# Optimization experiments

Measured on AMD Instinct MI355X. Metric: run time of the kernel, lower is better.

Reference implementation:

```python
import jax, jax.numpy as jnp
import numpy as np

HIDDEN = 512
OUTPUT = 256
TIMESTEPS = 16
THRESH = 0.5


def setup_inputs() -> dict:
    key = jax.random.key(0)
    k_x, k_w1, k_b1, k_w2, k_b2 = jax.random.split(key, 5)
    B, S, IN = 16, 2048, 512
    x = jax.random.normal(k_x, (B, S, IN), dtype=jnp.float32)
    # nn.Linear default init: U(-1/sqrt(fan_in), 1/sqrt(fan_in))
    lim1 = 1.0 / np.sqrt(IN)
    W1 = jax.random.uniform(k_w1, (HIDDEN, IN), minval=-lim1, maxval=lim1, dtype=jnp.float32)
    b1 = jax.random.uniform(k_b1, (HIDDEN,), minval=-lim1, maxval=lim1, dtype=jnp.float32)
    lim2 = 1.0 / np.sqrt(HIDDEN)
    W2 = jax.random.uniform(k_w2, (OUTPUT, HIDDEN), minval=-lim2, maxval=lim2, dtype=jnp.float32)
    b2 = jax.random.uniform(k_b2, (OUTPUT,), minval=-lim2, maxval=lim2, dtype=jnp.float32)
    return {"x": x, "W1": W1, "b1": b1, "W2": W2, "b2": b2}


def reference(x, W1, b1, W2, b2):
    # fc1(x) is the same every timestep (x is constant) -> compute once.
    pre1 = jnp.einsum("bsi,hi->bsh", x, W1) + b1  # [B,S,H]
    B, S, _ = pre1.shape
    mem1 = jnp.zeros((B, S, HIDDEN), dtype=x.dtype)
    mem2 = jnp.zeros((B, S, OUTPUT), dtype=x.dtype)
    spike_sum = jnp.zeros((B, S, OUTPUT), dtype=x.dtype)

    def step(carry, _):
        mem1, mem2, acc = carry
        mem1 = mem1 + pre1
        spike1 = (mem1 > THRESH).astype(x.dtype)
        mem1 = mem1 * (mem1 <= THRESH).astype(x.dtype)
        # dropout p=0.0 -> identity
        mem2 = mem2 + jnp.einsum("bsh,oh->bso", spike1, W2) + b2
        spike2 = (mem2 > THRESH).astype(x.dtype)
        mem2 = mem2 * (mem2 <= THRESH).astype(x.dtype)
        return (mem1, mem2, acc + spike2), None

    (mem1, mem2, spike_sum), _ = jax.lax.scan(
        step, (mem1, mem2, spike_sum), None, length=TIMESTEPS
    )
    return spike_sum / TIMESTEPS  # mean over timesteps, [B,S,OUTPUT]
```

## Files before the change

### kernel.cpp

```cpp
#include <hip/hip_runtime.h>
#include <cstdint>

#define NPOS 32768
#define IND  512
#define HID  512
#define OUTF 256

typedef float v2f __attribute__((ext_vector_type(2)));

__global__ __launch_bounds__(256) void k_transpose(const float* __restrict__ W2,
                                                   float* __restrict__ w2t) {
  __shared__ float tile[32][33];
  int x = threadIdx.x & 31, y = threadIdx.x >> 5;
  int hb = blockIdx.x * 32, ob = blockIdx.y * 32;
#pragma unroll
  for (int dy = 0; dy < 32; dy += 8)
    tile[y + dy][x] = W2[(size_t)(ob + y + dy) * HID + hb + x];
  __syncthreads();
#pragma unroll
  for (int dy = 0; dy < 32; dy += 8)
    w2t[(size_t)(hb + y + dy) * OUTF + ob + x] = tile[x][y + dy];
}

__global__ __launch_bounds__(256) void k_fc1_kmap(const float* __restrict__ X,
                                                  const float* __restrict__ W1,
                                                  const float* __restrict__ b1,
                                                  unsigned char* __restrict__ kmap) {
  __shared__ float As[8][128];
  __shared__ float Bs[8][128];
  const int row0 = blockIdx.x * 128;
  const int col0 = blockIdx.y * 128;
  const int t = threadIdx.x;
  const int tm0 = (t & 15) * 8;
  const int tn0 = (t >> 4) * 8;

  float c[8][8];
#pragma unroll
  for (int i = 0; i < 8; ++i)
#pragma unroll
    for (int j = 0; j < 8; ++j) c[i][j] = 0.0f;

  const int sm = t >> 1;
  const int sk = (t & 1) * 4;

  for (int kt = 0; kt < IND; kt += 8) {
    float4 va = *(const float4*)(X + (size_t)(row0 + sm) * IND + kt + sk);
    float4 vb = *(const float4*)(W1 + (size_t)(col0 + sm) * IND + kt + sk);
    __syncthreads();
    As[sk + 0][sm] = va.x; As[sk + 1][sm] = va.y;
    As[sk + 2][sm] = va.z; As[sk + 3][sm] = va.w;
    Bs[sk + 0][sm] = vb.x; Bs[sk + 1][sm] = vb.y;
    Bs[sk + 2][sm] = vb.z; Bs[sk + 3][sm] = vb.w;
    __syncthreads();
#pragma unroll
    for (int kk = 0; kk < 8; ++kk) {
      float4 a0 = *(const float4*)&As[kk][tm0];
      float4 a1 = *(const float4*)&As[kk][tm0 + 4];
      float4 b0 = *(const float4*)&Bs[kk][tn0];
      float4 b1_ = *(const float4*)&Bs[kk][tn0 + 4];
      float a[8] = {a0.x, a0.y, a0.z, a0.w, a1.x, a1.y, a1.z, a1.w};
      float b[8] = {b0.x, b0.y, b0.z, b0.w, b1_.x, b1_.y, b1_.z, b1_.w};
#pragma unroll
      for (int i = 0; i < 8; ++i)
#pragma unroll
        for (int j = 0; j < 8; ++j)
          c[i][j] = __fadd_rn(c[i][j], __fmul_rn(a[i], b[j]));
    }
  }

  float4 b1a = *(const float4*)(b1 + col0 + tn0);
  float4 b1b = *(const float4*)(b1 + col0 + tn0 + 4);
  float b1v[8] = {b1a.x, b1a.y, b1a.z, b1a.w, b1b.x, b1b.y, b1b.z, b1b.w};

#pragma unroll
  for (int i = 0; i < 8; ++i) {
    unsigned long long pk = 0;
#pragma unroll
    for (int j = 0; j < 8; ++j) {
      float pre = __fadd_rn(c[i][j], b1v[j]);
      float m = 0.0f;
      int kv = 0;
#pragma unroll
      for (int tt = 1; tt <= 16; ++tt) {
        m = __fadd_rn(m, pre);
        if (m > 0.5f && kv == 0) kv = tt;
      }
      pk |= (unsigned long long)(unsigned int)kv << (8 * j);
    }
    *(unsigned long long*)(kmap + (size_t)(row0 + tm0 + i) * HID + col0 + tn0) = pk;
  }
}

__global__ __launch_bounds__(128) void k_snn_fc2(const unsigned char* __restrict__ kmap,
                                                 const float* __restrict__ w2t,
                                                 const float* __restrict__ b2,
                                                 float* __restrict__ out) {
  const int tid = threadIdx.x;
  const size_t pos = blockIdx.x;

  v2f a1 = {0.f, 0.f}, a2 = a1, a3 = a1, a4 = a1, a5 = a1, a6 = a1,
      a7 = a1, a8 = a1, a9 = a1, a10 = a1, a11 = a1, a12 = a1,
      a13 = a1, a14 = a1, a15 = a1, a16 = a1;

  const uint4* kp = (const uint4*)(kmap + pos * HID);
  const v2f* w2p = (const v2f*)w2t;

#define PK(acc) asm volatile("v_pk_add_f32 %0, %0, %1" : "+v"(acc) : "v"(w))

#define DO_H(HB, KB)                                                      \
  do {                                                                    \
    int k_ = (int)(KB);                                                   \
    if (k_) {                                                             \
      v2f w = w2p[(size_t)(HB) * 128 + tid];                              \
      switch (k_) {                                                       \
        case 1:                                                           \
          PK(a1);  PK(a2);  PK(a3);  PK(a4);                              \
          PK(a5);  PK(a6);  PK(a7);  PK(a8);                              \
          PK(a9);  PK(a10); PK(a11); PK(a12);                             \
          PK(a13); PK(a14); PK(a15); PK(a16);                             \
          break;                                                          \
        case 2:                                                           \
          PK(a2);  PK(a4);  PK(a6);  PK(a8);                              \
          PK(a10); PK(a12); PK(a14); PK(a16);                             \
          break;                                                          \
        case 3:  PK(a3); PK(a6); PK(a9); PK(a12); PK(a15); break;         \
        case 4:  PK(a4); PK(a8); PK(a12); PK(a16); break;                 \
        case 5:  PK(a5); PK(a10); PK(a15); break;                         \
        case 6:  PK(a6); PK(a12); break;                                  \
        case 7:  PK(a7); PK(a14); break;                                  \
        case 8:  PK(a8); PK(a16); break;                                  \
        case 9:  PK(a9); break;                                           \
        case 10: PK(a10); break;                                          \
        case 11: PK(a11); break;                                          \
        case 12: PK(a12); break;                                          \
        case 13: PK(a13); break;                                          \
        case 14: PK(a14); break;                                          \
        case 15: PK(a15); break;                                          \
        default: PK(a16); break;                             \
      }                                                                   \
    }                                                                     \
  } while (0)

  for (int it = 0; it < 32; ++it) {
    uint4 kw = kp[it];
    int hb = it * 16;
    {
      unsigned uw = __builtin_amdgcn_readfirstlane(kw.x);
      DO_H(hb + 0, uw & 255u);         DO_H(hb + 1, (uw >> 8) & 255u);
      DO_H(hb + 2, (uw >> 16) & 255u); DO_H(hb + 3, uw >> 24);
    }
    {
      unsigned uw = __builtin_amdgcn_readfirstlane(kw.y);
      DO_H(hb + 4, uw & 255u);         DO_H(hb + 5, (uw >> 8) & 255u);
      DO_H(hb + 6, (uw >> 16) & 255u); DO_H(hb + 7, uw >> 24);
    }
    {
      unsigned uw = __builtin_amdgcn_readfirstlane(kw.z);
      DO_H(hb + 8, uw & 255u);          DO_H(hb + 9, (uw >> 8) & 255u);
      DO_H(hb + 10, (uw >> 16) & 255u); DO_H(hb + 11, uw >> 24);
    }
    {
      unsigned uw = __builtin_amdgcn_readfirstlane(kw.w);
      DO_H(hb + 12, uw & 255u);         DO_H(hb + 13, (uw >> 8) & 255u);
      DO_H(hb + 14, (uw >> 16) & 255u); DO_H(hb + 15, uw >> 24);
    }
  }
#undef DO_H
#undef PK

  v2f b2v = *(const v2f*)(b2 + 2 * tid);
  float memx = 0.0f, ssx = 0.0f, memy = 0.0f, ssy = 0.0f;
#define STEP(AT)                                              \
  do {                                                        \
    memx = __fadd_rn(__fadd_rn(memx, (AT).x), b2v.x);         \
    if (memx > 0.5f) { ssx += 1.0f; memx = 0.0f; }            \
    memy = __fadd_rn(__fadd_rn(memy, (AT).y), b2v.y);         \
    if (memy > 0.5f) { ssy += 1.0f; memy = 0.0f; }            \
  } while (0)
  STEP(a1);  STEP(a2);  STEP(a3);  STEP(a4);
  STEP(a5);  STEP(a6);  STEP(a7);  STEP(a8);
  STEP(a9);  STEP(a10); STEP(a11); STEP(a12);
  STEP(a13); STEP(a14); STEP(a15); STEP(a16);
#undef STEP
  v2f r = {ssx * 0.0625f, ssy * 0.0625f};
  *(v2f*)(out + pos * OUTF + 2 * tid) = r;
}

extern "C" void kernel_launch(void* const* d_in, const int* in_sizes, int n_in,
                              void* d_out, int out_size, void* d_ws, size_t ws_size,
                              hipStream_t stream) {
  const float* X  = (const float*)d_in[0];
  const float* W1 = (const float*)d_in[1];
  const float* b1 = (const float*)d_in[2];
  const float* W2 = (const float*)d_in[3];
  const float* b2 = (const float*)d_in[4];
  float* out = (float*)d_out;

  float* w2t = (float*)d_ws;
  unsigned char* kmap = (unsigned char*)d_ws + (size_t)HID * OUTF * 4;

  k_transpose<<<dim3(16, 8), 256, 0, stream>>>(W2, w2t);
  k_fc1_kmap<<<dim3(256, 4), 256, 0, stream>>>(X, W1, b1, kmap);
  k_snn_fc2<<<NPOS, 128, 0, stream>>>(kmap, w2t, b2, out);
}
```

Before: 1.461 ms.

## Stage W2 chunks in LDS shared by eight positions per block

The fc2 spike-accumulation kernel now handles eight positions per 512-thread block, one wave per position, with each lane covering four outputs. W2^T is staged into shared memory in 64-row chunks so the eight waves reuse it instead of each re-reading it from global or L2. This adds block-wide barriers and a 64KB LDS footprint, which limits occupancy, and it doubles the accumulator registers per lane.

```diff
diff --git a/kernel.cpp b/kernel.cpp
--- a/kernel.cpp
+++ b/kernel.cpp
@@ -91,99 +91,130 @@
   }
 }
 
-__global__ __launch_bounds__(128) void k_snn_fc2(const unsigned char* __restrict__ kmap,
+__global__ __launch_bounds__(512) void k_snn_fc2(const unsigned char* __restrict__ kmap,
                                                  const float* __restrict__ w2t,
                                                  const float* __restrict__ b2,
                                                  float* __restrict__ out) {
+  __shared__ float w2s[64 * 256];
   const int tid = threadIdx.x;
-  const size_t pos = blockIdx.x;
-
-  v2f a1 = {0.f, 0.f}, a2 = a1, a3 = a1, a4 = a1, a5 = a1, a6 = a1,
-      a7 = a1, a8 = a1, a9 = a1, a10 = a1, a11 = a1, a12 = a1,
-      a13 = a1, a14 = a1, a15 = a1, a16 = a1;
-
-  const uint4* kp = (const uint4*)(kmap + pos * HID);
-  const v2f* w2p = (const v2f*)w2t;
-
-#define PK(acc) asm volatile("v_pk_add_f32 %0, %0, %1" : "+v"(acc) : "v"(w))
-
-#define DO_H(HB, KB)                                                      \
+  const int wave = tid >> 6;
+  const int lane = tid & 63;
+  const size_t pos = (size_t)blockIdx.x * 8 + wave;
+
+  v2f z = {0.f, 0.f};
+  v2f a1l = z, a2l = z, a3l = z, a4l = z, a5l = z, a6l = z, a7l = z, a8l = z,
+      a9l = z, a10l = z, a11l = z, a12l = z, a13l = z, a14l = z, a15l = z, a16l = z;
+  v2f a1h = z, a2h = z, a3h = z, a4h = z, a5h = z, a6h = z, a7h = z, a8h = z,
+      a9h = z, a10h = z, a11h = z, a12h = z, a13h = z, a14h = z, a15h = z, a16h = z;
+
+  const v2f* wp = (const v2f*)w2s;
+
+#define PK2(accl, acch)                                                   \
+  do {                                                                    \
+    asm volatile("v_pk_add_f32 %0, %0, %1" : "+v"(accl) : "v"(wlo));      \
+    asm volatile("v_pk_add_f32 %0, %0, %1" : "+v"(acch) : "v"(whi));      \
+  } while (0)
+
+#define DO_H(HL, KB)                                                      \
   do {                                                                    \
     int k_ = (int)(KB);                                                   \
     if (k_) {                                                             \
-      v2f w = w2p[(size_t)(HB) * 128 + tid];                              \
+      v2f wlo = wp[(HL) * 128 + lane * 2];                                \
+      v2f whi = wp[(HL) * 128 + lane * 2 + 1];                            \
       switch (k_) {                                                       \
         case 1:                                                           \
-          PK(a1);  PK(a2);  PK(a3);  PK(a4);                              \
-          PK(a5);  PK(a6);  PK(a7);  PK(a8);                              \
-          PK(a9);  PK(a10); PK(a11); PK(a12);                             \
-          PK(a13); PK(a14); PK(a15); PK(a16);                             \
+          PK2(a1l, a1h);  PK2(a2l, a2h);  PK2(a3l, a3h);  PK2(a4l, a4h);  \
+          PK2(a5l, a5h);  PK2(a6l, a6h);  PK2(a7l, a7h);  PK2(a8l, a8h);  \
+          PK2(a9l, a9h);  PK2(a10l, a10h); PK2(a11l, a11h); PK2(a12l, a12h);\
+          PK2(a13l, a13h); PK2(a14l, a14h); PK2(a15l, a15h); PK2(a16l, a16h);\
           break;                                                          \
         case 2:                                                           \
-          PK(a2);  PK(a4);  PK(a6);  PK(a8);                              \
-          PK(a10); PK(a12); PK(a14); PK(a16);                             \
+          PK2(a2l, a2h);  PK2(a4l, a4h);  PK2(a6l, a6h);  PK2(a8l, a8h);  \
+          PK2(a10l, a10h); PK2(a12l, a12h); PK2(a14l, a14h); PK2(a16l, a16h);\
           break;                                                          \
-        case 3:  PK(a3); PK(a6); PK(a9); PK(a12); PK(a15); break;         \
-        case 4:  PK(a4); PK(a8); PK(a12); PK(a16); break;                 \
-        case 5:  PK(a5); PK(a10); PK(a15); break;                         \
-        case 6:  PK(a6); PK(a12); break;                                  \
-        case 7:  PK(a7); PK(a14); break;                                  \
-        case 8:  PK(a8); PK(a16); break;                                  \
-        case 9:  PK(a9); break;                                           \
-        case 10: PK(a10); break;                                          \
-        case 11: PK(a11); break;                                          \
-        case 12: PK(a12); break;                                          \
-        case 13: PK(a13); break;                                          \
-        case 14: PK(a14); break;                                          \
-        case 15: PK(a15); break;                                          \
-        default: PK(a16); break;                             \
+        case 3:                                                           \
+          PK2(a3l, a3h); PK2(a6l, a6h); PK2(a9l, a9h); PK2(a12l, a12h);   \
+          PK2(a15l, a15h); break;                                         \
+        case 4:                                                           \
+          PK2(a4l, a4h); PK2(a8l, a8h); PK2(a12l, a12h); PK2(a16l, a16h); \
+          break;                                                          \
+        case 5:  PK2(a5l, a5h); PK2(a10l, a10h); PK2(a15l, a15h); break;  \
+        case 6:  PK2(a6l, a6h); PK2(a12l, a12h); break;                   \
+        case 7:  PK2(a7l, a7h); PK2(a14l, a14h); break;                   \
+        case 8:  PK2(a8l, a8h); PK2(a16l, a16h); break;                   \
+        case 9:  PK2(a9l, a9h); break;                                    \
+        case 10: PK2(a10l, a10h); break;                                  \
+        case 11: PK2(a11l, a11h); break;                                  \
+        case 12: PK2(a12l, a12h); break;                                  \
+        case 13: PK2(a13l, a13h); break;                                  \
+        case 14: PK2(a14l, a14h); break;                                  \
+        case 15: PK2(a15l, a15h); break;                                  \
+        default: PK2(a16l, a16h); break;                     \
       }                                                                   \
     }                                                                     \
   } while (0)
 
-  for (int it = 0; it < 32; ++it) {
-    uint4 kw = kp[it];
-    int hb = it * 16;
-    {
-      unsigned uw = __builtin_amdgcn_readfirstlane(kw.x);
-      DO_H(hb + 0, uw & 255u);         DO_H(hb + 1, (uw >> 8) & 255u);
-      DO_H(hb + 2, (uw >> 16) & 255u); DO_H(hb + 3, uw >> 24);
-    }
-    {
-      unsigned uw = __builtin_amdgcn_readfirstlane(kw.y);
-      DO_H(hb + 4, uw & 255u);         DO_H(hb + 5, (uw >> 8) & 255u);
-      DO_H(hb + 6, (uw >> 16) & 255u); DO_H(hb + 7, uw >> 24);
-    }
-    {
-      unsigned uw = __builtin_amdgcn_readfirstlane(kw.z);
-      DO_H(hb + 8, uw & 255u);          DO_H(hb + 9, (uw >> 8) & 255u);
-      DO_H(hb + 10, (uw >> 16) & 255u); DO_H(hb + 11, uw >> 24);
-    }
-    {
-      unsigned uw = __builtin_amdgcn_readfirstlane(kw.w);
-      DO_H(hb + 12, uw & 255u);         DO_H(hb + 13, (uw >> 8) & 255u);
-      DO_H(hb + 14, (uw >> 16) & 255u); DO_H(hb + 15, uw >> 24);
+  for (int ch = 0; ch < 8; ++ch) {
+    __syncthreads();
+    const float4* src = (const float4*)(w2t + (size_t)ch * 64 * 256);
+#pragma unroll
+    for (int j = 0; j < 8; ++j) {
+      int fi = tid + j * 512;
+      ((float4*)w2s)[fi] = src[fi];
+    }
+    __syncthreads();
+
+    const uint4* kp = (const uint4*)(kmap + pos * HID + ch * 64);
+#pragma unroll
+    for (int q = 0; q < 4; ++q) {
+      uint4 kw = kp[q];
+      int hl = q * 16;
+      {
+        unsigned uw = __builtin_amdgcn_readfirstlane(kw.x);
+        DO_H(hl + 0, uw & 255u);         DO_H(hl + 1, (uw >> 8) & 255u);
+        DO_H(hl + 2, (uw >> 16) & 255u); DO_H(hl + 3, uw >> 24);
+      }
+      {
+        unsigned uw = __builtin_amdgcn_readfirstlane(kw.y);
+        DO_H(hl + 4, uw & 255u);         DO_H(hl + 5, (uw >> 8) & 255u);
+        DO_H(hl + 6, (uw >> 16) & 255u); DO_H(hl + 7, uw >> 24);
+      }
+      {
+        unsigned uw = __builtin_amdgcn_readfirstlane(kw.z);
+        DO_H(hl + 8, uw & 255u);          DO_H(hl + 9, (uw >> 8) & 255u);
+        DO_H(hl + 10, (uw >> 16) & 255u); DO_H(hl + 11, uw >> 24);
+      }
+      {
+        unsigned uw = __builtin_amdgcn_readfirstlane(kw.w);
+        DO_H(hl + 12, uw & 255u);         DO_H(hl + 13, (uw >> 8) & 255u);
+        DO_H(hl + 14, (uw >> 16) & 255u); DO_H(hl + 15, uw >> 24);
+      }
     }
   }
 #undef DO_H
-#undef PK
-
-  v2f b2v = *(const v2f*)(b2 + 2 * tid);
-  float memx = 0.0f, ssx = 0.0f, memy = 0.0f, ssy = 0.0f;
-#define STEP(AT)                                              \
+#undef PK2
+
+  float4 b2v = *(const float4*)(b2 + 4 * lane);
+  float m0 = 0.f, m1 = 0.f, m2 = 0.f, m3 = 0.f;
+  float s0 = 0.f, s1 = 0.f, s2 = 0.f, s3 = 0.f;
+#define STEP(AL, AH)                                          \
   do {                                                        \
-    memx = __fadd_rn(__fadd_rn(memx, (AT).x), b2v.x);         \
-    if (memx > 0.5f) { ssx += 1.0f; memx = 0.0f; }            \
-    memy = __fadd_rn(__fadd_rn(memy, (AT).y), b2v.y);         \
-    if (memy > 0.5f) { ssy += 1.0f; memy = 0.0f; }            \
+    m0 = __fadd_rn(__fadd_rn(m0, (AL).x), b2v.x);             \
+    if (m0 > 0.5f) { s0 += 1.0f; m0 = 0.0f; }                 \
+    m1 = __fadd_rn(__fadd_rn(m1, (AL).y), b2v.y);             \
+    if (m1 > 0.5f) { s1 += 1.0f; m1 = 0.0f; }                 \
+    m2 = __fadd_rn(__fadd_rn(m2, (AH).x), b2v.z);             \
+    if (m2 > 0.5f) { s2 += 1.0f; m2 = 0.0f; }                 \
+    m3 = __fadd_rn(__fadd_rn(m3, (AH).y), b2v.w);             \
+    if (m3 > 0.5f) { s3 += 1.0f; m3 = 0.0f; }                 \
   } while (0)
-  STEP(a1);  STEP(a2);  STEP(a3);  STEP(a4);
-  STEP(a5);  STEP(a6);  STEP(a7);  STEP(a8);
-  STEP(a9);  STEP(a10); STEP(a11); STEP(a12);
-  STEP(a13); STEP(a14); STEP(a15); STEP(a16);
+  STEP(a1l, a1h);   STEP(a2l, a2h);   STEP(a3l, a3h);   STEP(a4l, a4h);
+  STEP(a5l, a5h);   STEP(a6l, a6h);   STEP(a7l, a7h);   STEP(a8l, a8h);
+  STEP(a9l, a9h);   STEP(a10l, a10h); STEP(a11l, a11h); STEP(a12l, a12h);
+  STEP(a13l, a13h); STEP(a14l, a14h); STEP(a15l, a15h); STEP(a16l, a16h);
 #undef STEP
-  v2f r = {ssx * 0.0625f, ssy * 0.0625f};
-  *(v2f*)(out + pos * OUTF + 2 * tid) = r;
+  float4 r = make_float4(s0 * 0.0625f, s1 * 0.0625f, s2 * 0.0625f, s3 * 0.0625f);
+  *(float4*)(out + pos * OUTF + 4 * lane) = r;
 }
 
 extern "C" void kernel_launch(void* const* d_in, const int* in_sizes, int n_in,
@@ -201,5 +232,5 @@
 
   k_transpose<<<dim3(16, 8), 256, 0, stream>>>(W2, w2t);
   k_fc1_kmap<<<dim3(256, 4), 256, 0, stream>>>(X, W1, b1, kmap);
-  k_snn_fc2<<<NPOS, 128, 0, stream>>>(kmap, w2t, b2, out);
-}
+  k_snn_fc2<<<NPOS / 8, 512, 0, stream>>>(kmap, w2t, b2, out);
+}
```

Result: slower. 2.025 ms (+38.6%).
